# Optimization experiments

Measured on AMD Instinct MI355X. Metric: run time of the kernel, lower is better.

## Reference

```python
import jax, jax.numpy as jnp
import numpy as np

B, S, D, H = 2, 2048, 1024, 8
DH = D // H          # hidden_dim == attn_dim == 128
TOTAL = 4 * D        # (2*hidden_dim + 2*attn_dim) * H
EPS = 1e-5
ROPE_BASE = 10000.0


def _layernorm(x, g, b):
    m = jnp.mean(x, axis=-1, keepdims=True)
    v = jnp.mean(jnp.square(x - m), axis=-1, keepdims=True)
    return (x - m) * jax.lax.rsqrt(v + EPS) * g + b


def _rope(x):
    # x: [B, H, S, DH], interleaved even/odd RoPE as in the torch module
    half = DH // 2
    inv_freq = 1.0 / (ROPE_BASE ** (jnp.arange(0, DH, 2, dtype=jnp.float32) / DH))  # [half]
    t = jnp.arange(x.shape[2], dtype=jnp.float32)
    freqs = t[:, None] * inv_freq[None, :]                 # [S, half]
    cos = jnp.cos(freqs)[None, None, :, :]                 # [1,1,S,half]
    sin = jnp.sin(freqs)[None, None, :, :]
    xe, xo = x[..., 0::2], x[..., 1::2]
    re = xe * cos - xo * sin
    ro = xe * sin + xo * cos
    return jnp.stack([re, ro], axis=-1).reshape(x.shape)


def setup_inputs() -> dict:
    key = jax.random.key(0)
    ks = jax.random.split(key, 6)
    x = jax.random.normal(ks[0], (B, S, D), dtype=jnp.float32)
    attention_mask = jnp.ones((B, S), dtype=bool)
    # weights stored [in, out] so forward is x @ W + b
    w_uvqk = 0.02 * jax.random.normal(ks[1], (D, TOTAL), dtype=jnp.float32)
    b_uvqk = jnp.zeros((TOTAL,), dtype=jnp.float32)
    w_out = 0.02 * jax.random.normal(ks[2], (3 * D, D), dtype=jnp.float32)
    b_out = jnp.zeros((D,), dtype=jnp.float32)
    ln1_g = jnp.ones((D,), dtype=jnp.float32)
    ln1_b = jnp.zeros((D,), dtype=jnp.float32)
    ln2_g = jnp.ones((D,), dtype=jnp.float32)
    ln2_b = jnp.zeros((D,), dtype=jnp.float32)
    return {"x": x, "attention_mask": attention_mask,
            "ln1_g": ln1_g, "ln1_b": ln1_b,
            "w_uvqk": w_uvqk, "b_uvqk": b_uvqk,
            "ln2_g": ln2_g, "ln2_b": ln2_b,
            "w_out": w_out, "b_out": b_out}


def reference(x, attention_mask, ln1_g, ln1_b, w_uvqk, b_uvqk, ln2_g, ln2_b, w_out, b_out):
    normed = _layernorm(x, ln1_g, ln1_b)
    uvqk = jax.nn.silu(normed @ w_uvqk + b_uvqk)          # [B,S,4D]
    u, v, q, k = jnp.split(uvqk, [D, 2 * D, 3 * D], axis=-1)
    q = q.reshape(B, S, H, DH).transpose(0, 2, 1, 3)      # [B,H,S,DH]
    k = k.reshape(B, S, H, DH).transpose(0, 2, 1, 3)
    v = v.reshape(B, S, H, DH).transpose(0, 2, 1, 3)
    q, k = _rope(q), _rope(k)
    scale = jnp.float32(DH) ** 0.5
    scores = jnp.einsum('bhsd,bhtd->bhst', q, k) / scale  # [B,H,S,S] fp32
    causal = jnp.tril(jnp.ones((S, S), dtype=bool))
    pad = attention_mask[:, None, :, None] & attention_mask[:, None, None, :]
    valid = pad & causal[None, None, :, :]
    scores = jnp.where(valid, scores, jnp.float32(-30.0))
    scores = jnp.clip(scores, -30.0, 30.0)
    attn = jax.nn.silu(scores)                            # SiLU instead of softmax
    ao = jnp.einsum('bhst,bhtd->bhsd', attn, v)           # [B,H,S,DH]
    ao = ao.transpose(0, 2, 1, 3).reshape(B, S, D)
    normed_attn = _layernorm(ao, ln2_g, ln2_b)
    cat = jnp.concatenate([u, ao, normed_attn * u], axis=-1)  # [B,S,3D]
    return x + (cat @ w_out + b_out)
```

## Files before the change

kernel.cpp:

```cpp
#include <hip/hip_runtime.h>
#include <hip/hip_bf16.h>
#include <math.h>

#define Bm 2
#define Sm 2048
#define Dm 1024
#define Hm 8
#define DHm 128
#define TOTALm 4096
#define ROWS (Bm*Sm)
#define K2m (3*Dm)

typedef __bf16 bf16;
typedef __bf16 bf16x8 __attribute__((ext_vector_type(8)));
typedef __bf16 bf16x4 __attribute__((ext_vector_type(4)));
typedef float  f32x4  __attribute__((ext_vector_type(4)));

__device__ __forceinline__ void stage_tile_128x32(
    const bf16* __restrict__ g, int ld, bf16* lds, int tid)
{
    int wid = tid >> 6;
    #pragma unroll
    for (int j = 0; j < 2; j++) {
        int e0  = (j*256 + tid) * 8;
        int row = e0 >> 5, col = e0 & 31;
        const bf16* src = g + (size_t)row*ld + col;
        bf16* dst = lds + (size_t)(j*256 + wid*64)*8;
        __builtin_amdgcn_global_load_lds(
            (const __attribute__((address_space(1))) unsigned int*)src,
            (__attribute__((address_space(3))) unsigned int*)dst,
            16, 0, 0);
    }
}

__device__ __forceinline__ void stage_tile_64x32(
    const bf16* __restrict__ g, int ld, bf16* lds, int tid)
{
    int wid = tid >> 6;
    int e0 = tid * 8;
    int row = e0 >> 5, col = e0 & 31;
    const bf16* src = g + (size_t)row*ld + col;
    bf16* dst = lds + (size_t)wid*512;
    __builtin_amdgcn_global_load_lds(
        (const __attribute__((address_space(1))) unsigned int*)src,
        (__attribute__((address_space(3))) unsigned int*)dst,
        16, 0, 0);
}

__global__ __launch_bounds__(256) void ln1_kernel(
    const float* __restrict__ x, const float* __restrict__ g,
    const float* __restrict__ bb, bf16* __restrict__ out)
{
    int row = blockIdx.x;
    const float* xr = x + (size_t)row * Dm;
    int tid = threadIdx.x;
    float4 v = *(const float4*)(xr + tid*4);
    float s = v.x+v.y+v.z+v.w;
    for (int o=32;o>0;o>>=1) s += __shfl_down(s,o);
    __shared__ float red[4]; __shared__ float stats[2];
    int wid = tid>>6, lane = tid&63;
    if (lane==0) red[wid]=s;
    __syncthreads();
    if (tid==0) stats[0] = (red[0]+red[1]+red[2]+red[3]) * (1.f/Dm);
    __syncthreads();
    float m = stats[0];
    float d0=v.x-m,d1=v.y-m,d2=v.z-m,d3=v.w-m;
    float q = d0*d0+d1*d1+d2*d2+d3*d3;
    for (int o=32;o>0;o>>=1) q += __shfl_down(q,o);
    if (lane==0) red[wid]=q;
    __syncthreads();
    if (tid==0) stats[1] = rsqrtf((red[0]+red[1]+red[2]+red[3])*(1.f/Dm) + 1e-5f);
    __syncthreads();
    float rs = stats[1];
    float4 gv = *(const float4*)(g + tid*4);
    float4 bv = *(const float4*)(bb + tid*4);
    bf16x4 o;
    o[0] = (bf16)(d0*rs*gv.x + bv.x);
    o[1] = (bf16)(d1*rs*gv.y + bv.y);
    o[2] = (bf16)(d2*rs*gv.z + bv.z);
    o[3] = (bf16)(d3*rs*gv.w + bv.w);
    *(bf16x4*)(out + (size_t)row*Dm + tid*4) = o;
}

__global__ __launch_bounds__(256) void transpose_kernel(
    const float* __restrict__ in, bf16* __restrict__ out, int R, int C)
{
    __shared__ float tile[32][33];
    int c0 = blockIdx.x*32, r0 = blockIdx.y*32;
    int tx = threadIdx.x & 31, ty = threadIdx.x >> 5;
    for (int i=0;i<4;i++) {
        int r = ty + i*8;
        tile[r][tx] = in[(size_t)(r0+r)*C + c0+tx];
    }
    __syncthreads();
    for (int i=0;i<4;i++) {
        int cl = ty + i*8;
        out[(size_t)(c0+cl)*R + r0+tx] = (bf16)tile[tx][cl];
    }
}

__global__ __launch_bounds__(256) void rope_table_kernel(float* __restrict__ ct, float* __restrict__ st)
{
    int idx = blockIdx.x*256 + threadIdx.x;
    int t = idx >> 6, p = idx & 63;
    float inv = expf(-0.143911568f * (float)p);
    float f = (float)t * inv;
    float sv, cv;
    sincosf(f, &sv, &cv);
    ct[idx] = cv; st[idx] = sv;
}

__global__ __launch_bounds__(256,4) void gemm1_kernel(
    const bf16* __restrict__ A, const bf16* __restrict__ Bt,
    const float* __restrict__ bias,
    const float* __restrict__ ct, const float* __restrict__ st,
    bf16* __restrict__ cat, bf16* __restrict__ qb, bf16* __restrict__ kb,
    bf16* __restrict__ vt)
{
    __shared__ __align__(16) bf16 sm[17408];
    const int K = Dm;
    int m0 = blockIdx.y*128, n0 = blockIdx.x*128;
    int tid = threadIdx.x, wid = tid>>6, lane = tid&63;
    int quad = lane>>4, l16 = lane&15;
    int wm = (wid>>1)*64, wn = (wid&1)*64;
    f32x4 acc[4][4] = {};
    bf16* sA = sm;
    bf16* sB = sm + 8192;
    for (int k0=0;k0<K;k0+=64) {
        __syncthreads();
        stage_tile_128x32(A  + (size_t)m0*K + k0,      K, sA,        tid);
        stage_tile_128x32(A  + (size_t)m0*K + k0 + 32, K, sA + 4096, tid);
        stage_tile_128x32(Bt + (size_t)n0*K + k0,      K, sB,        tid);
        stage_tile_128x32(Bt + (size_t)n0*K + k0 + 32, K, sB + 4096, tid);
        __syncthreads();
        #pragma unroll
        for (int kc=0;kc<2;kc++) {
            bf16x8 af[4], bfr[4];
            #pragma unroll
            for (int t=0;t<4;t++) af[t]  = *(const bf16x8*)&sA[kc*4096 + (wm+t*16+l16)*32 + quad*8];
            #pragma unroll
            for (int t=0;t<4;t++) bfr[t] = *(const bf16x8*)&sB[kc*4096 + (wn+t*16+l16)*32 + quad*8];
            #pragma unroll
            for (int tm=0;tm<4;tm++)
                #pragma unroll
                for (int tn=0;tn<4;tn++)
                    acc[tm][tn] = __builtin_amdgcn_mfma_f32_16x16x32_bf16(af[tm], bfr[tn], acc[tm][tn], 0,0,0);
        }
    }
    int sect = n0 >> 10;
    if (sect == 1) {
        __syncthreads();
        #pragma unroll
        for (int tm=0;tm<4;tm++)
        #pragma unroll
        for (int tn=0;tn<4;tn++) {
            int colg = n0 + wn + tn*16 + l16;
            float bval = bias[colg];
            int d = colg & 127;
            #pragma unroll
            for (int r=0;r<4;r++) {
                int srow = wm + tm*16 + quad*4 + r;
                float val = acc[tm][tn][r] + bval;
                val = val / (1.f + __expf(-val));
                sm[d*136 + srow] = (bf16)val;
            }
        }
        __syncthreads();
        int h = (n0 >> 7) & 7;
        int b = m0 >> 11, s0l = m0 & 2047;
        int d2 = tid >> 1, sh = (tid & 1)*64;
        bf16* dst = vt + ((size_t)(b*Hm+h)*DHm + d2)*Sm + s0l + sh;
        const bf16* srcl = &sm[d2*136 + sh];
        #pragma unroll
        for (int i=0;i<8;i++)
            *(bf16x8*)(dst + i*8) = *(const bf16x8*)(srcl + i*8);
    } else if (sect == 0) {
        #pragma unroll
        for (int tm=0;tm<4;tm++)
        #pragma unroll
        for (int tn=0;tn<4;tn++) {
            int c = n0 + wn + tn*16 + l16;
            float bval = bias[c];
            #pragma unroll
            for (int r=0;r<4;r++) {
                int row = m0 + wm + tm*16 + quad*4 + r;
                float val = acc[tm][tn][r] + bval;
                val = val / (1.f + __expf(-val));
                cat[(size_t)row*K2m + c] = (bf16)val;
            }
        }
    } else {
        bf16* dstb = (sect==2) ? qb : kb;
        float postscale = (sect==2) ? 0.08838834764831845f : 1.0f;
        #pragma unroll
        for (int tm=0;tm<4;tm++)
        #pragma unroll
        for (int tn=0;tn<4;tn++) {
            int colg = n0 + wn + tn*16 + l16;
            int c = colg & 1023;
            int h = c>>7, d = c&127, p = d>>1;
            float bval = bias[colg];
            #pragma unroll
            for (int r=0;r<4;r++) {
                int row = m0 + wm + tm*16 + quad*4 + r;
                float val = acc[tm][tn][r] + bval;
                val = val / (1.f + __expf(-val));
                int b = row>>11, s = row&2047;
                float pv = __shfl_xor(val, 1);
                float cv = ct[s*64+p], sv = st[s*64+p];
                float res = (d&1) ? (pv*sv + val*cv) : (val*cv - pv*sv);
                dstb[((size_t)(b*Hm+h)*Sm + s)*DHm + d] = (bf16)(res * postscale);
            }
        }
    }
}

__global__ __launch_bounds__(256,3) void attn_kernel(
    const bf16* __restrict__ qb, const bf16* __restrict__ kb,
    const bf16* __restrict__ vt, float* __restrict__ ao0,
    float* __restrict__ ao1)
{
    __shared__ __align__(16) bf16 P[2*64*136];
    int bid = blockIdx.x;
    int head = bid & 15;
    int idx = bid >> 4;
    int b = head >> 3, h = head & 7;
    int qt, k_begin, k_end;
    float* aoOut;
    if (idx < 32) {
        qt = 31 - (idx >> 1);
        int nkt = (qt >> 1) + 1;
        int half = (nkt + 1) >> 1;
        if ((idx & 1) == 0) { k_begin = 0;    k_end = half; aoOut = ao0; }
        else                { k_begin = half; k_end = nkt;  aoOut = ao1; }
    } else {
        qt = 47 - idx;
        k_begin = 0; k_end = (qt >> 1) + 1;
        aoOut = ao0;
    }
    const size_t headoff = (size_t)(b*Hm+h)*Sm*DHm;
    const bf16* Q  = qb + headoff;
    const bf16* Km = kb + headoff;
    const bf16* V  = vt + headoff;
    int tid=threadIdx.x, wid=tid>>6, lane=tid&63, quad=lane>>4, l16=lane&15;
    int wm=(wid>>1)*32, wn=(wid&1)*64;
    int q0 = qt*64;
    f32x4 accO[2][4] = {};
    bf16x8 qf[4][2];
    #pragma unroll
    for (int kc=0;kc<4;kc++)
        #pragma unroll
        for (int t=0;t<2;t++)
            qf[kc][t] = *(const bf16x8*)(Q + (size_t)(q0+wm+t*16+l16)*DHm + kc*32 + quad*8);
    int it = 0;
    for (int kt=k_begin; kt<k_end; kt++, it++) {
        int t0 = kt*128;
        bf16* Pb = P + (it & 1) * 8704;
        f32x4 accS[2][4] = {};
        #pragma unroll
        for (int kc=0;kc<4;kc++) {
            bf16x8 bfr[4];
            #pragma unroll
            for (int t=0;t<4;t++)
                bfr[t] = *(const bf16x8*)(Km + (size_t)(t0+wn+t*16+l16)*DHm + kc*32 + quad*8);
            #pragma unroll
            for (int tm=0;tm<2;tm++)
                #pragma unroll
                for (int tn=0;tn<4;tn++)
                    accS[tm][tn] = __builtin_amdgcn_mfma_f32_16x16x32_bf16(qf[kc][tm], bfr[tn], accS[tm][tn], 0,0,0);
        }
        if (t0 + 127 <= q0) {
            #pragma unroll
            for (int tm=0;tm<2;tm++)
            #pragma unroll
            for (int tn=0;tn<4;tn++)
                #pragma unroll
                for (int r=0;r<4;r++) {
                    int srow = wm+tm*16+quad*4+r;
                    int tcol = wn+tn*16+l16;
                    float s = fminf(30.f, fmaxf(-30.f, accS[tm][tn][r]));
                    float p = s * __builtin_amdgcn_rcpf(1.f + __expf(-s));
                    Pb[srow*136 + tcol] = (bf16)p;
                }
        } else {
            #pragma unroll
            for (int tm=0;tm<2;tm++)
            #pragma unroll
            for (int tn=0;tn<4;tn++)
                #pragma unroll
                for (int r=0;r<4;r++) {
                    int srow = wm+tm*16+quad*4+r;
                    int tcol = wn+tn*16+l16;
                    float s = fminf(30.f, fmaxf(-30.f, accS[tm][tn][r]));
                    float p = (t0+tcol > q0+srow) ? 0.f
                              : s * __builtin_amdgcn_rcpf(1.f + __expf(-s));
                    Pb[srow*136 + tcol] = (bf16)p;
                }
        }
        __syncthreads();
        int kcn = ((q0 + 63 - t0) >> 5) + 1;
        if (kcn > 4) kcn = 4;
        for (int kc=0;kc<kcn;kc++) {
            bf16x8 af[2], bfr[4];
            #pragma unroll
            for (int t=0;t<2;t++) af[t]  = *(const bf16x8*)&Pb[(wm+t*16+l16)*136 + kc*32 + quad*8];
            #pragma unroll
            for (int t=0;t<4;t++) bfr[t] = *(const bf16x8*)(V + (size_t)(wn+t*16+l16)*Sm + t0 + kc*32 + quad*8);
            #pragma unroll
            for (int tm=0;tm<2;tm++)
                #pragma unroll
                for (int tn=0;tn<4;tn++)
                    accO[tm][tn] = __builtin_amdgcn_mfma_f32_16x16x32_bf16(af[tm], bfr[tn], accO[tm][tn], 0,0,0);
        }
    }
    #pragma unroll
    for (int tm=0;tm<2;tm++)
    #pragma unroll
    for (int tn=0;tn<4;tn++)
        #pragma unroll
        for (int r=0;r<4;r++) {
            int s = q0+wm+tm*16+quad*4+r;
            int d = wn+tn*16+l16;
            aoOut[((size_t)(b*Sm+s))*Dm + h*DHm + d] = accO[tm][tn][r];
        }
}

__global__ __launch_bounds__(256) void ln2_cat_kernel(
    const float* __restrict__ ao0, const float* __restrict__ ao1,
    const float* __restrict__ g,
    const float* __restrict__ bb, bf16* __restrict__ cat)
{
    int row = blockIdx.x;
    int tid = threadIdx.x;
    float4 v  = *(const float4*)(ao0 + (size_t)row*Dm + tid*4);
    float4 v1 = *(const float4*)(ao1 + (size_t)row*Dm + tid*4);
    v.x += v1.x; v.y += v1.y; v.z += v1.z; v.w += v1.w;
    float s = v.x+v.y+v.z+v.w;
    for (int o=32;o>0;o>>=1) s += __shfl_down(s,o);
    __shared__ float red[4]; __shared__ float stats[2];
    int wid = tid>>6, lane = tid&63;
    if (lane==0) red[wid]=s;
    __syncthreads();
    if (tid==0) stats[0] = (red[0]+red[1]+red[2]+red[3]) * (1.f/Dm);
    __syncthreads();
    float m = stats[0];
    float d0=v.x-m,d1=v.y-m,d2=v.z-m,d3=v.w-m;
    float q = d0*d0+d1*d1+d2*d2+d3*d3;
    for (int o=32;o>0;o>>=1) q += __shfl_down(q,o);
    if (lane==0) red[wid]=q;
    __syncthreads();
    if (tid==0) stats[1] = rsqrtf((red[0]+red[1]+red[2]+red[3])*(1.f/Dm) + 1e-5f);
    __syncthreads();
    float rs = stats[1];
    float4 gv = *(const float4*)(g + tid*4);
    float4 bv = *(const float4*)(bb + tid*4);
    bf16* crow = cat + (size_t)row * K2m;
    bf16x4 u4 = *(const bf16x4*)(crow + tid*4);
    bf16x4 a4, nu4;
    a4[0]=(bf16)v.x; a4[1]=(bf16)v.y; a4[2]=(bf16)v.z; a4[3]=(bf16)v.w;
    nu4[0]=(bf16)(((v.x-m)*rs*gv.x+bv.x) * (float)u4[0]);
    nu4[1]=(bf16)(((v.y-m)*rs*gv.y+bv.y) * (float)u4[1]);
    nu4[2]=(bf16)(((v.z-m)*rs*gv.z+bv.z) * (float)u4[2]);
    nu4[3]=(bf16)(((v.w-m)*rs*gv.w+bv.w) * (float)u4[3]);
    *(bf16x4*)(crow + 1024 + tid*4) = a4;
    *(bf16x4*)(crow + 2048 + tid*4) = nu4;
}

__global__ __launch_bounds__(256,4) void gemm2_kernel(
    const bf16* __restrict__ A, const bf16* __restrict__ Bt,
    const float* __restrict__ bias, const float* __restrict__ x,
    float* __restrict__ out)
{
    __shared__ __align__(16) bf16 sm[12288];
    const int K = K2m, N = Dm;
    int m0 = blockIdx.y*128, n0 = blockIdx.x*64;
    int tid = threadIdx.x, wid = tid>>6, lane = tid&63;
    int quad = lane>>4, l16 = lane&15;
    int wm = (wid>>1)*64, wn = (wid&1)*32;
    f32x4 acc[4][2] = {};
    bf16* sA = sm;
    bf16* sB = sm + 8192;
    for (int k0=0;k0<K;k0+=64) {
        __syncthreads();
        stage_tile_128x32(A  + (size_t)m0*K + k0,      K, sA,        tid);
        stage_tile_128x32(A  + (size_t)m0*K + k0 + 32, K, sA + 4096, tid);
        stage_tile_64x32 (Bt + (size_t)n0*K + k0,      K, sB,        tid);
        stage_tile_64x32 (Bt + (size_t)n0*K + k0 + 32, K, sB + 2048, tid);
        __syncthreads();
        #pragma unroll
        for (int kc=0;kc<2;kc++) {
            bf16x8 af[4], bfr[2];
            #pragma unroll
            for (int t=0;t<4;t++) af[t]  = *(const bf16x8*)&sA[kc*4096 + (wm+t*16+l16)*32 + quad*8];
            #pragma unroll
            for (int t=0;t<2;t++) bfr[t] = *(const bf16x8*)&sB[kc*2048 + (wn+t*16+l16)*32 + quad*8];
            #pragma unroll
            for (int tm=0;tm<4;tm++)
                #pragma unroll
                for (int tn=0;tn<2;tn++)
                    acc[tm][tn] = __builtin_amdgcn_mfma_f32_16x16x32_bf16(af[tm], bfr[tn], acc[tm][tn], 0,0,0);
        }
    }
    #pragma unroll
    for (int tm=0;tm<4;tm++)
    #pragma unroll
    for (int tn=0;tn<2;tn++) {
        int col = n0 + wn + tn*16 + l16;
        float bval = bias[col];
        #pragma unroll
        for (int r=0;r<4;r++) {
            int row = m0 + wm + tm*16 + quad*4 + r;
            out[(size_t)row*N + col] = acc[tm][tn][r] + bval + x[(size_t)row*N + col];
        }
    }
}

extern "C" void kernel_launch(void* const* d_in, const int* in_sizes, int n_in,
                              void* d_out, int out_size, void* d_ws, size_t ws_size,
                              hipStream_t stream)
{
    const float* x      = (const float*)d_in[0];
    const float* ln1_g  = (const float*)d_in[2];
    const float* ln1_b  = (const float*)d_in[3];
    const float* w_uvqk = (const float*)d_in[4];
    const float* b_uvqk = (const float*)d_in[5];
    const float* ln2_g  = (const float*)d_in[6];
    const float* ln2_b  = (const float*)d_in[7];
    const float* w_out  = (const float*)d_in[8];
    const float* b_out  = (const float*)d_in[9];

    char* w = (char*)d_ws;
    bf16*  normed = (bf16*)(w);
    bf16*  Wt1    = (bf16*)(w + 8388608);
    bf16*  Wt2    = (bf16*)(w + 16777216);
    bf16*  qb     = (bf16*)(w + 23068672);
    bf16*  kb     = (bf16*)(w + 31457280);
    bf16*  vt     = (bf16*)(w + 39845888);
    float* ao0    = (float*)(w + 48234496);
    bf16*  cat    = (bf16*)(w + 65011712);
    float* ct     = (float*)(w + 90177536);
    float* st     = (float*)(w + 90701824);
    float* ao1    = (float*)(w);

    ln1_kernel<<<ROWS, 256, 0, stream>>>(x, ln1_g, ln1_b, normed);
    transpose_kernel<<<dim3(TOTALm/32, Dm/32), 256, 0, stream>>>(w_uvqk, Wt1, Dm, TOTALm);
    transpose_kernel<<<dim3(Dm/32, K2m/32), 256, 0, stream>>>(w_out, Wt2, K2m, Dm);
    rope_table_kernel<<<(Sm*64)/256, 256, 0, stream>>>(ct, st);
    gemm1_kernel<<<dim3(TOTALm/128, ROWS/128), 256, 0, stream>>>(
        normed, Wt1, b_uvqk, ct, st, cat, qb, kb, vt);
    hipMemsetAsync(ao1, 0, (size_t)ROWS*Dm*sizeof(float), stream);
    attn_kernel<<<768, 256, 0, stream>>>(qb, kb, vt, ao0, ao1);
    ln2_cat_kernel<<<ROWS, 256, 0, stream>>>(ao0, ao1, ln2_g, ln2_b, cat);
    gemm2_kernel<<<dim3(Dm/64, ROWS/128), 256, 0, stream>>>(
        cat, Wt2, b_out, x, (float*)d_out);
}
```

Measured before the change: 300.8 us.

## Stage K tiles through LDS with register prefetch and hoist V loads

The attention kernel now loads each 128-row K tile cooperatively into shared memory, prefetching the next tile into registers while the current one is consumed. Previously each wave read K fragments straight from global memory, duplicating traffic across waves. V fragments for the whole tile are loaded early so their latency overlaps the QK^T MFMAs and SiLU, and the P buffer drops from double to single buffering. The extra registers and LDS cut the occupancy hint from 3 to 2 blocks per CU, and an extra barrier per tile is added.

```diff
diff --git a/kernel.cpp b/kernel.cpp
--- a/kernel.cpp
+++ b/kernel.cpp
@@ -215,12 +215,13 @@
     }
 }
 
-__global__ __launch_bounds__(256,3) void attn_kernel(
+__global__ __launch_bounds__(256,2) void attn_kernel(
     const bf16* __restrict__ qb, const bf16* __restrict__ kb,
     const bf16* __restrict__ vt, float* __restrict__ ao0,
     float* __restrict__ ao1)
 {
-    __shared__ __align__(16) bf16 P[2*64*136];
+    __shared__ __align__(16) bf16 sK[16384];
+    __shared__ __align__(16) bf16 P[64*136];
     int bid = blockIdx.x;
     int head = bid & 15;
     int idx = bid >> 4;
@@ -252,17 +253,47 @@
         #pragma unroll
         for (int t=0;t<2;t++)
             qf[kc][t] = *(const bf16x8*)(Q + (size_t)(q0+wm+t*16+l16)*DHm + kc*32 + quad*8);
-    int it = 0;
-    for (int kt=k_begin; kt<k_end; kt++, it++) {
+    int e0 = tid*8, e1 = (256+tid)*8;
+    int kr0 = e0>>5, kcol0 = e0&31;
+    int kr1 = e1>>5, kcol1 = e1&31;
+    bf16x8 kreg[4][2];
+    {
+        int t0 = k_begin*128;
+        #pragma unroll
+        for (int kc=0;kc<4;kc++) {
+            kreg[kc][0] = *(const bf16x8*)(Km + (size_t)(t0+kr0)*DHm + kc*32 + kcol0);
+            kreg[kc][1] = *(const bf16x8*)(Km + (size_t)(t0+kr1)*DHm + kc*32 + kcol1);
+        }
+    }
+    for (int kt=k_begin; kt<k_end; kt++) {
         int t0 = kt*128;
-        bf16* Pb = P + (it & 1) * 8704;
+        __syncthreads();
+        #pragma unroll
+        for (int kc=0;kc<4;kc++) {
+            *(bf16x8*)&sK[kc*4096 + e0] = kreg[kc][0];
+            *(bf16x8*)&sK[kc*4096 + e1] = kreg[kc][1];
+        }
+        __syncthreads();
+        if (kt+1 < k_end) {
+            int t0n = t0 + 128;
+            #pragma unroll
+            for (int kc=0;kc<4;kc++) {
+                kreg[kc][0] = *(const bf16x8*)(Km + (size_t)(t0n+kr0)*DHm + kc*32 + kcol0);
+                kreg[kc][1] = *(const bf16x8*)(Km + (size_t)(t0n+kr1)*DHm + kc*32 + kcol1);
+            }
+        }
+        bf16x8 vreg[4][4];
+        #pragma unroll
+        for (int kc=0;kc<4;kc++)
+            #pragma unroll
+            for (int t=0;t<4;t++)
+                vreg[kc][t] = *(const bf16x8*)(V + (size_t)(wn+t*16+l16)*Sm + t0 + kc*32 + quad*8);
         f32x4 accS[2][4] = {};
         #pragma unroll
         for (int kc=0;kc<4;kc++) {
             bf16x8 bfr[4];
             #pragma unroll
-            for (int t=0;t<4;t++)
-                bfr[t] = *(const bf16x8*)(Km + (size_t)(t0+wn+t*16+l16)*DHm + kc*32 + quad*8);
+            for (int t=0;t<4;t++) bfr[t] = *(const bf16x8*)&sK[kc*4096 + (wn+t*16+l16)*32 + quad*8];
             #pragma unroll
             for (int tm=0;tm<2;tm++)
                 #pragma unroll
@@ -280,7 +311,7 @@
                     int tcol = wn+tn*16+l16;
                     float s = fminf(30.f, fmaxf(-30.f, accS[tm][tn][r]));
                     float p = s * __builtin_amdgcn_rcpf(1.f + __expf(-s));
-                    Pb[srow*136 + tcol] = (bf16)p;
+                    P[srow*136 + tcol] = (bf16)p;
                 }
         } else {
             #pragma unroll
@@ -294,23 +325,23 @@
                     float s = fminf(30.f, fmaxf(-30.f, accS[tm][tn][r]));
                     float p = (t0+tcol > q0+srow) ? 0.f
                               : s * __builtin_amdgcn_rcpf(1.f + __expf(-s));
-                    Pb[srow*136 + tcol] = (bf16)p;
+                    P[srow*136 + tcol] = (bf16)p;
                 }
         }
         __syncthreads();
         int kcn = ((q0 + 63 - t0) >> 5) + 1;
         if (kcn > 4) kcn = 4;
-        for (int kc=0;kc<kcn;kc++) {
-            bf16x8 af[2], bfr[4];
-            #pragma unroll
-            for (int t=0;t<2;t++) af[t]  = *(const bf16x8*)&Pb[(wm+t*16+l16)*136 + kc*32 + quad*8];
-            #pragma unroll
-            for (int t=0;t<4;t++) bfr[t] = *(const bf16x8*)(V + (size_t)(wn+t*16+l16)*Sm + t0 + kc*32 + quad*8);
+        #pragma unroll
+        for (int kc=0;kc<4;kc++) {
+            if (kc >= kcn) break;
+            bf16x8 af[2];
+            #pragma unroll
+            for (int t=0;t<2;t++) af[t] = *(const bf16x8*)&P[(wm+t*16+l16)*136 + kc*32 + quad*8];
             #pragma unroll
             for (int tm=0;tm<2;tm++)
                 #pragma unroll
                 for (int tn=0;tn<4;tn++)
-                    accO[tm][tn] = __builtin_amdgcn_mfma_f32_16x16x32_bf16(af[tm], bfr[tn], accO[tm][tn], 0,0,0);
+                    accO[tm][tn] = __builtin_amdgcn_mfma_f32_16x16x32_bf16(af[tm], vreg[kc][tn], accO[tm][tn], 0,0,0);
         }
     }
     #pragma unroll
```

New measurement: 283.4 us. 5.8% less time.

## Restructure attention into per-wave register-resident strips and drop the ao1 memset

Applied to the files above, without the earlier changes.

Each wave now owns a 32-row query strip for one head and computes the transposed score tile, K times Q. The SiLU probabilities then land in registers already laid out as the B operand of a 16x16x16 MFMA for the PV product. This removes the LDS P buffer and the block-wide barrier. The causal key range of each strip is split into two segments that write ao0 and ao1 in full, zeros included, so the ao1 memset is no longer needed. In exchange, K and V tiles are fetched from global memory by each wave with less reuse (32 query rows per load instead of 64), and occupancy is lowered to 2 blocks per SM.

```diff
diff --git a/kernel.cpp b/kernel.cpp
--- a/kernel.cpp
+++ b/kernel.cpp
@@ -15,6 +15,17 @@
 typedef __bf16 bf16x8 __attribute__((ext_vector_type(8)));
 typedef __bf16 bf16x4 __attribute__((ext_vector_type(4)));
 typedef float  f32x4  __attribute__((ext_vector_type(4)));
+typedef short  s16x4  __attribute__((ext_vector_type(4)));
+
+__device__ __forceinline__ f32x4 mfma_16x16x16_bf16(bf16x4 a, bf16x4 b, f32x4 c)
+{
+#if __has_builtin(__builtin_amdgcn_mfma_f32_16x16x16_bf16)
+    return __builtin_amdgcn_mfma_f32_16x16x16_bf16(a, b, c, 0, 0, 0);
+#else
+    return __builtin_amdgcn_mfma_f32_16x16x16bf16_1k(
+        __builtin_bit_cast(s16x4, a), __builtin_bit_cast(s16x4, b), c, 0, 0, 0);
+#endif
+}
 
 __device__ __forceinline__ void stage_tile_128x32(
     const bf16* __restrict__ g, int ld, bf16* lds, int tid)
@@ -215,113 +226,94 @@
     }
 }
 
-__global__ __launch_bounds__(256,3) void attn_kernel(
+__global__ __launch_bounds__(256,2) void attn_kernel(
     const bf16* __restrict__ qb, const bf16* __restrict__ kb,
     const bf16* __restrict__ vt, float* __restrict__ ao0,
     float* __restrict__ ao1)
 {
-    __shared__ __align__(16) bf16 P[2*64*136];
-    int bid = blockIdx.x;
-    int head = bid & 15;
-    int idx = bid >> 4;
+    int tid = threadIdx.x;
+    int wid = tid>>6, lane = tid&63, quad = lane>>4, l16 = lane&15;
+    int gid = blockIdx.x*4 + wid;
+    int head = gid & 15;
+    int r = gid >> 4;
+    int seg   = (r < 64) ? 0 : 1;
+    int strip = (r < 64) ? r : (127 - r);
     int b = head >> 3, h = head & 7;
-    int qt, k_begin, k_end;
-    float* aoOut;
-    if (idx < 32) {
-        qt = 31 - (idx >> 1);
-        int nkt = (qt >> 1) + 1;
-        int half = (nkt + 1) >> 1;
-        if ((idx & 1) == 0) { k_begin = 0;    k_end = half; aoOut = ao0; }
-        else                { k_begin = half; k_end = nkt;  aoOut = ao1; }
-    } else {
-        qt = 47 - idx;
-        k_begin = 0; k_end = (qt >> 1) + 1;
-        aoOut = ao0;
-    }
+    int s0 = strip * 32;
+    int nt = (strip >> 1) + 1;
+    int half = (nt + 1) >> 1;
+    int t_begin = seg ? half : 0;
+    int t_end   = seg ? nt   : half;
+    float* aoOut = seg ? ao1 : ao0;
     const size_t headoff = (size_t)(b*Hm+h)*Sm*DHm;
     const bf16* Q  = qb + headoff;
     const bf16* Km = kb + headoff;
     const bf16* V  = vt + headoff;
-    int tid=threadIdx.x, wid=tid>>6, lane=tid&63, quad=lane>>4, l16=lane&15;
-    int wm=(wid>>1)*32, wn=(wid&1)*64;
-    int q0 = qt*64;
-    f32x4 accO[2][4] = {};
-    bf16x8 qf[4][2];
+
+    bf16x8 qf[2][4];
     #pragma unroll
-    for (int kc=0;kc<4;kc++)
-        #pragma unroll
-        for (int t=0;t<2;t++)
-            qf[kc][t] = *(const bf16x8*)(Q + (size_t)(q0+wm+t*16+l16)*DHm + kc*32 + quad*8);
-    int it = 0;
-    for (int kt=k_begin; kt<k_end; kt++, it++) {
-        int t0 = kt*128;
-        bf16* Pb = P + (it & 1) * 8704;
-        f32x4 accS[2][4] = {};
-        #pragma unroll
-        for (int kc=0;kc<4;kc++) {
-            bf16x8 bfr[4];
-            #pragma unroll
-            for (int t=0;t<4;t++)
-                bfr[t] = *(const bf16x8*)(Km + (size_t)(t0+wn+t*16+l16)*DHm + kc*32 + quad*8);
-            #pragma unroll
-            for (int tm=0;tm<2;tm++)
+    for (int st=0; st<2; st++)
+        #pragma unroll
+        for (int kc=0; kc<4; kc++)
+            qf[st][kc] = *(const bf16x8*)(Q + (size_t)(s0+st*16+l16)*DHm + kc*32 + quad*8);
+
+    f32x4 accO[8][2] = {};
+
+    for (int ti = t_begin; ti < t_end; ti++) {
+        int t0 = ti*64;
+        f32x4 accS[4][2] = {};
+        #pragma unroll
+        for (int kc=0; kc<4; kc++) {
+            bf16x8 kf[4];
+            #pragma unroll
+            for (int ts=0; ts<4; ts++)
+                kf[ts] = *(const bf16x8*)(Km + (size_t)(t0+ts*16+l16)*DHm + kc*32 + quad*8);
+            #pragma unroll
+            for (int ts=0; ts<4; ts++)
                 #pragma unroll
-                for (int tn=0;tn<4;tn++)
-                    accS[tm][tn] = __builtin_amdgcn_mfma_f32_16x16x32_bf16(qf[kc][tm], bfr[tn], accS[tm][tn], 0,0,0);
-        }
-        if (t0 + 127 <= q0) {
-            #pragma unroll
-            for (int tm=0;tm<2;tm++)
-            #pragma unroll
-            for (int tn=0;tn<4;tn++)
+                for (int st=0; st<2; st++)
+                    accS[ts][st] = __builtin_amdgcn_mfma_f32_16x16x32_bf16(
+                        kf[ts], qf[st][kc], accS[ts][st], 0,0,0);
+        }
+        bool clean = (t0 + 63 <= s0);
+        bf16x4 pb[4][2];
+        #pragma unroll
+        for (int ts=0; ts<4; ts++)
+            #pragma unroll
+            for (int st=0; st<2; st++) {
                 #pragma unroll
-                for (int r=0;r<4;r++) {
-                    int srow = wm+tm*16+quad*4+r;
-                    int tcol = wn+tn*16+l16;
-                    float s = fminf(30.f, fmaxf(-30.f, accS[tm][tn][r]));
-                    float p = s * __builtin_amdgcn_rcpf(1.f + __expf(-s));
-                    Pb[srow*136 + tcol] = (bf16)p;
+                for (int rr=0; rr<4; rr++) {
+                    float sc = accS[ts][st][rr];
+                    sc = fminf(30.f, fmaxf(-30.f, sc));
+                    float p = sc * __builtin_amdgcn_rcpf(1.f + __expf(-sc));
+                    if (!clean) {
+                        int tg = t0 + ts*16 + quad*4 + rr;
+                        int sg = s0 + st*16 + l16;
+                        if (tg > sg) p = 0.f;
+                    }
+                    pb[ts][st][rr] = (bf16)p;
                 }
-        } else {
-            #pragma unroll
-            for (int tm=0;tm<2;tm++)
-            #pragma unroll
-            for (int tn=0;tn<4;tn++)
+            }
+        #pragma unroll
+        for (int ts=0; ts<4; ts++) {
+            bf16x4 vf[8];
+            #pragma unroll
+            for (int dt=0; dt<8; dt++)
+                vf[dt] = *(const bf16x4*)(V + (size_t)(dt*16+l16)*Sm + t0 + ts*16 + quad*4);
+            #pragma unroll
+            for (int dt=0; dt<8; dt++)
                 #pragma unroll
-                for (int r=0;r<4;r++) {
-                    int srow = wm+tm*16+quad*4+r;
-                    int tcol = wn+tn*16+l16;
-                    float s = fminf(30.f, fmaxf(-30.f, accS[tm][tn][r]));
-                    float p = (t0+tcol > q0+srow) ? 0.f
-                              : s * __builtin_amdgcn_rcpf(1.f + __expf(-s));
-                    Pb[srow*136 + tcol] = (bf16)p;
-                }
-        }
-        __syncthreads();
-        int kcn = ((q0 + 63 - t0) >> 5) + 1;
-        if (kcn > 4) kcn = 4;
-        for (int kc=0;kc<kcn;kc++) {
-            bf16x8 af[2], bfr[4];
-            #pragma unroll
-            for (int t=0;t<2;t++) af[t]  = *(const bf16x8*)&Pb[(wm+t*16+l16)*136 + kc*32 + quad*8];
-            #pragma unroll
-            for (int t=0;t<4;t++) bfr[t] = *(const bf16x8*)(V + (size_t)(wn+t*16+l16)*Sm + t0 + kc*32 + quad*8);
-            #pragma unroll
-            for (int tm=0;tm<2;tm++)
-                #pragma unroll
-                for (int tn=0;tn<4;tn++)
-                    accO[tm][tn] = __builtin_amdgcn_mfma_f32_16x16x32_bf16(af[tm], bfr[tn], accO[tm][tn], 0,0,0);
+                for (int st=0; st<2; st++)
+                    accO[dt][st] = mfma_16x16x16_bf16(vf[dt], pb[ts][st], accO[dt][st]);
         }
     }
     #pragma unroll
-    for (int tm=0;tm<2;tm++)
-    #pragma unroll
-    for (int tn=0;tn<4;tn++)
-        #pragma unroll
-        for (int r=0;r<4;r++) {
-            int s = q0+wm+tm*16+quad*4+r;
-            int d = wn+tn*16+l16;
-            aoOut[((size_t)(b*Sm+s))*Dm + h*DHm + d] = accO[tm][tn][r];
+    for (int dt=0; dt<8; dt++)
+        #pragma unroll
+        for (int st=0; st<2; st++) {
+            float* dst = aoOut + ((size_t)(b*Sm + s0 + st*16 + l16))*Dm
+                       + h*DHm + dt*16 + quad*4;
+            *(float4*)dst = *(float4*)&accO[dt][st];
         }
 }
 
@@ -448,8 +440,7 @@
     rope_table_kernel<<<(Sm*64)/256, 256, 0, stream>>>(ct, st);
     gemm1_kernel<<<dim3(TOTALm/128, ROWS/128), 256, 0, stream>>>(
         normed, Wt1, b_uvqk, ct, st, cat, qb, kb, vt);
-    hipMemsetAsync(ao1, 0, (size_t)ROWS*Dm*sizeof(float), stream);
-    attn_kernel<<<768, 256, 0, stream>>>(qb, kb, vt, ao0, ao1);
+    attn_kernel<<<512, 256, 0, stream>>>(qb, kb, vt, ao0, ao1);
     ln2_cat_kernel<<<ROWS, 256, 0, stream>>>(ao0, ao1, ln2_g, ln2_b, cat);
     gemm2_kernel<<<dim3(Dm/64, ROWS/128), 256, 0, stream>>>(
         cat, Wt2, b_out, x, (float*)d_out);
```

After: 358.9 us. 19.3% more time.
